# Optimization experiments

Hardware: AMD Instinct MI355X
Metric: run time of the kernel (lower is better)

Reference implementation:

```python
import jax, jax.numpy as jnp
import numpy as np
from jax import lax

N_CLASS = 20
N_BOX = 2
GRID = 56          # n_cell_hw derived from input width: 56*56*(2*5+20) = 94080
BATCH = 256
SCORE_THRESH = 0.1 # hard-coded in _preds_filte
IOU_THRESH = 0.4   # hard-coded in _preds_filte
MAX_OUT = 30       # max_output_size
NMS_CAND = 256     # pre-select top candidates per image before O(K^2) NMS


def setup_inputs() -> dict:
    key = jax.random.key(0)
    D = GRID * GRID * (N_BOX * 5 + N_CLASS)
    net_outs = jax.random.uniform(key, (BATCH, D), dtype=jnp.float32)
    return {"net_outs": net_outs}


def _decode(net_outs):
    # Faithful port of _net_outs_parse (wh_sqrt=True)
    B = net_outs.shape[0]
    S, nb, C = GRID, N_BOX, N_CLASS
    bd1 = C * S * S
    bd2 = bd1 + nb * S * S
    cell_c = net_outs[:, :bd1].reshape(B, S, S, C)
    conf = net_outs[:, bd1:bd2].reshape(B, S, S, nb)
    coord = net_outs[:, bd2:].reshape(B, S, S, nb, 4)
    t_xy, t_wh = coord[..., :2], coord[..., 2:]
    # mesh_grid: w_index varies along axis 1, h_index along axis 0, stacked as (w, h)
    X, Y = jnp.meshgrid(jnp.arange(S, dtype=net_outs.dtype),
                        jnp.arange(S, dtype=net_outs.dtype), indexing='xy')
    grid = jnp.stack([X, Y], axis=-1)[:, :, None, :]  # [S,S,1,2]
    xy = (t_xy + grid) / S
    wh = jnp.square(t_wh)  # wh_sqrt=True
    mn = xy - wh * 0.5
    mx = xy + wh * 0.5
    # boxes_corner = [ymin, xmin, ymax, xmax]
    corners = jnp.concatenate([mn[..., 1:2], mn[..., 0:1], mx[..., 1:2], mx[..., 0:1]], axis=-1)
    c_probs = jnp.broadcast_to(cell_c[:, :, :, None, :], (B, S, S, nb, C))
    return jnp.concatenate([corners, conf[..., None], c_probs], axis=-1)  # [B,S,S,nb,5+C]


def _pairwise_iou(b):
    ymin, xmin, ymax, xmax = b[:, 0], b[:, 1], b[:, 2], b[:, 3]
    area = jnp.maximum(ymax - ymin, 0.0) * jnp.maximum(xmax - xmin, 0.0)
    iy = jnp.maximum(0.0, jnp.minimum(ymax[:, None], ymax[None, :]) - jnp.maximum(ymin[:, None], ymin[None, :]))
    ix = jnp.maximum(0.0, jnp.minimum(xmax[:, None], xmax[None, :]) - jnp.maximum(xmin[:, None], xmin[None, :]))
    inter = iy * ix
    union = area[:, None] + area[None, :] - inter
    return jnp.where(union > 0.0, inter / union, 0.0)


def _nms_image(item):
    # item: [N, 6] = (ymin, xmin, ymax, xmax, score, class)
    scores = item[:, 4]
    _, top_i = lax.top_k(scores, NMS_CAND)   # candidate pre-selection (greedy NMS only ever picks highest scores)
    cand = item[top_i]                       # [K, 6]
    iou = _pairwise_iou(cand[:, :4])         # [K, K]
    neg = jnp.finfo(item.dtype).min

    def step(valid, _):
        m = jnp.where(valid, cand[:, 4], neg)
        idx = jnp.argmax(m)
        ok = valid[idx]
        valid = valid & (iou[idx] <= IOU_THRESH)
        valid = valid.at[idx].set(False)
        return valid, (idx, ok)

    _, (idxs, ok) = lax.scan(step, jnp.ones(NMS_CAND, dtype=bool), None, length=MAX_OUT)
    rows = cand[idxs] * ok[:, None].astype(item.dtype)  # invalid slots -> zero rows (== pad with 0)
    _, oi = lax.top_k(rows[:, 4], MAX_OUT)               # sort by score desc, like tf.nn.top_k on padded preds
    return rows[oi]


def reference(net_outs):
    preds = _decode(net_outs)                    # [B,S,S,nb,25]
    B = preds.shape[0]
    cls_score = preds[..., 4:5] * preds[..., 5:]  # conf * class probs  [B,S,S,nb,C]
    cls = jnp.argmax(cls_score, axis=-1).astype(preds.dtype)
    s = jnp.max(cls_score, axis=-1)
    s = jnp.where(s >= SCORE_THRESH, s, 0.0)
    items = jnp.concatenate([preds[..., :4], s[..., None], cls[..., None]], axis=-1)
    items = items.reshape(B, -1, 6)              # [B, S*S*nb, 6]
    return jax.vmap(_nms_image)(items)           # [B, MAX_OUT, 6]
```

## Files before the change

### kernel.cpp

```cpp
#include <hip/hip_runtime.h>
#include <stdint.h>

#define S      56
#define NC     20
#define NCELL  (S*S)
#define NBOXES (NCELL*2)
#define DIM    94080
#define BD1    62720
#define BD2    68992
#define CAND   256
#define MAXOUT 30
#define NTHR   1024
#define NWAVE  16
#define NBIN   8192
#define CAP    512

__global__ __launch_bounds__(NTHR) void det_kernel(const float* __restrict__ in,
                                                   float* __restrict__ out) {
#pragma clang fp contract(off)
    const int b    = blockIdx.x;
    const int tid  = threadIdx.x;
    const int lane = tid & 63;
    const int wv   = tid >> 6;
    const float* img = in + (size_t)b * DIM;

    __shared__ uint32_t hist[NBIN];
    __shared__ uint32_t wsum[NWAVE];
    __shared__ int      bstar_s;
    __shared__ int      nsel;
    __shared__ uint64_t skey[CAP];
    __shared__ uint64_t ssort[CAND];
    __shared__ float cymin[CAND], cxmin[CAND], cymax[CAND], cxmax[CAND];
    __shared__ float carea[CAND], cscore[CAND], ccls[CAND];
    __shared__ int   klist[MAXOUT];
    __shared__ float rowbuf[MAXOUT * 6];

    ((uint4*)hist)[tid]        = uint4{0,0,0,0};
    ((uint4*)hist)[tid + NTHR] = uint4{0,0,0,0};
    if (tid == 0) nsel = 0;
    if (tid < MAXOUT) klist[tid] = -1;

    uint64_t key[4][2];
    bool     vld[4];
    #pragma unroll
    for (int i = 0; i < 4; i++) {
        int cell = tid + NTHR * i;
        vld[i] = (cell < NCELL);
        key[i][0] = key[i][1] = 0;
        if (vld[i]) {
            const float4* pv = (const float4*)(img + cell * NC);
            float p[NC];
            #pragma unroll
            for (int q = 0; q < 5; q++) {
                float4 v = pv[q];
                p[4*q+0] = v.x; p[4*q+1] = v.y; p[4*q+2] = v.z; p[4*q+3] = v.w;
            }
            float2 cf = *(const float2*)(img + BD1 + cell * 2);
            #pragma unroll
            for (int bb = 0; bb < 2; bb++) {
                float conf = bb ? cf.y : cf.x;
                float best = conf * p[0];
                int   cls  = 0;
                #pragma unroll
                for (int c = 1; c < NC; c++) {
                    float v = conf * p[c];
                    if (v > best) { best = v; cls = c; }
                }
                uint32_t sb = (best >= 0.1f) ? __float_as_uint(best) : 0u;
                int idx = cell * 2 + bb;
                key[i][bb] = ((uint64_t)sb << 18) | ((uint64_t)(8191 - idx) << 5)
                           | (uint64_t)cls;
            }
        }
    }
    __syncthreads();

    #pragma unroll
    for (int i = 0; i < 4; i++) {
        #pragma unroll
        for (int bb = 0; bb < 2; bb++) {
            uint32_t sb = (uint32_t)(key[i][bb] >> 18);
            if (vld[i] && sb != 0u) atomicAdd(&hist[sb >> 17], 1u);
            unsigned long long zm = __ballot(vld[i] && sb == 0u);
            if (lane == 0 && zm) atomicAdd(&hist[0], (uint32_t)__popcll(zm));
        }
    }
    __syncthreads();

    uint4 h0 = ((const uint4*)hist)[2*tid];
    uint4 h1 = ((const uint4*)hist)[2*tid+1];
    uint32_t hsum = h0.x+h0.y+h0.z+h0.w + h1.x+h1.y+h1.z+h1.w;
    uint32_t v = hsum;
    #pragma unroll
    for (int off = 1; off < 64; off <<= 1) {
        uint32_t u = __shfl_down(v, off);
        if (lane + off < 64) v += u;
    }
    if (lane == 0) wsum[wv] = v;
    __syncthreads();
    uint32_t add = 0;
    for (int w = wv + 1; w < NWAVE; w++) add += wsum[w];
    uint32_t Sm    = v + add;
    uint32_t above = Sm - hsum;
    if (above < CAND && CAND <= Sm) {
        uint32_t hh[8] = {h1.w, h1.z, h1.y, h1.x, h0.w, h0.z, h0.y, h0.x};
        uint32_t g = above;
        int bsel = 8 * tid;
        #pragma unroll
        for (int j = 0; j < 8; j++) {
            if (g + hh[j] >= CAND) { bsel = 8 * tid + (7 - j); break; }
            g += hh[j];
        }
        bstar_s = bsel;
    }
    __syncthreads();
    const uint32_t bstar = (uint32_t)bstar_s;

    #pragma unroll
    for (int i = 0; i < 4; i++) {
        #pragma unroll
        for (int bb = 0; bb < 2; bb++) {
            bool pred = vld[i] && ((uint32_t)(key[i][bb] >> 35) >= bstar);
            unsigned long long mask = __ballot(pred);
            if (mask) {
                int leader = __ffsll(mask) - 1;
                int base = 0;
                if (lane == leader) base = atomicAdd(&nsel, (int)__popcll(mask));
                base = __shfl(base, leader);
                if (pred) {
                    int pos = base + (int)__popcll(mask & ((1ull << lane) - 1ull));
                    if (pos < CAP) skey[pos] = key[i][bb];
                }
            }
        }
    }
    __syncthreads();

    const int M = (nsel < CAP) ? nsel : CAP;
    if (tid < M) {
        uint64_t my = skey[tid];
        int r = 0;
        #pragma unroll 4
        for (int j = 0; j < M; j++) r += (skey[j] > my);
        if (r < CAND) ssort[r] = my;
    }
    __syncthreads();

    if (tid < CAND) {
        uint64_t k = ssort[tid];
        int idx      = 8191 - (int)((k >> 5) & 0x1FFF);
        int cls      = (int)(k & 31u);
        uint32_t sb  = (uint32_t)(k >> 18);
        int cell = idx >> 1, bb = idx & 1;
        int i = cell / S, j = cell - i * S;
        float4 co = *(const float4*)(img + BD2 + cell * 8 + bb * 4);
        float x  = (co.x + (float)j) / 56.0f;
        float y  = (co.y + (float)i) / 56.0f;
        float wx = co.z * co.z;
        float wy = co.w * co.w;
        float hx = wx * 0.5f, hy = wy * 0.5f;
        float xmin = x - hx, ymin = y - hy, xmax = x + hx, ymax = y + hy;
        cymin[tid] = ymin; cxmin[tid] = xmin; cymax[tid] = ymax; cxmax[tid] = xmax;
        carea[tid] = fmaxf(ymax - ymin, 0.0f) * fmaxf(xmax - xmin, 0.0f);
        cscore[tid] = __uint_as_float(sb);
        ccls[tid]   = (float)cls;
    }
    __syncthreads();

    if (wv == 0) {
        float bym[4], bxm[4], byM[4], bxM[4], bar[4];
        #pragma unroll
        for (int s = 0; s < 4; s++) {
            int c = 4 * lane + s;
            bym[s] = cymin[c]; bxm[s] = cxmin[c];
            byM[s] = cymax[c]; bxM[s] = cxmax[c]; bar[s] = carea[c];
        }
        unsigned vmask = 0xFu;
        for (int it = 0; it < MAXOUT; it++) {
            unsigned long long mk = __ballot(vmask != 0u);
            if (!mk) break;
            int l0 = __ffsll(mk) - 1;
            int vb = __shfl((int)vmask, l0);
            int p  = 4 * l0 + (__ffs(vb) - 1);
            if (lane == 0) klist[it] = p;
            float pym = cymin[p], pxm = cxmin[p];
            float pyM = cymax[p], pxM = cxmax[p], par = carea[p];
            #pragma unroll
            for (int s = 0; s < 4; s++) {
                int c = 4 * lane + s;
                float iy = fmaxf(0.0f, fminf(pyM, byM[s]) - fmaxf(pym, bym[s]));
                float ix = fmaxf(0.0f, fminf(pxM, bxM[s]) - fmaxf(pxm, bxm[s]));
                float inter = iy * ix;
                float uni   = par + bar[s] - inter;
                float iou   = (uni > 0.0f) ? (inter / uni) : 0.0f;
                if (c == p || !(iou <= 0.4f)) vmask &= ~(1u << s);
            }
        }
    }
    __syncthreads();

    if (tid < MAXOUT) {
        int p = klist[tid];
        float* r = &rowbuf[tid * 6];
        if (p >= 0) {
            r[0] = cymin[p]; r[1] = cxmin[p]; r[2] = cymax[p];
            r[3] = cxmax[p]; r[4] = cscore[p]; r[5] = ccls[p];
        } else {
            r[0] = r[1] = r[2] = r[3] = r[4] = r[5] = 0.0f;
        }
    }
    __syncthreads();
    float* ob = out + (size_t)b * (MAXOUT * 6);
    if (tid < MAXOUT * 6) ob[tid] = rowbuf[tid];
}

extern "C" void kernel_launch(void* const* d_in, const int* in_sizes, int n_in,
                              void* d_out, int out_size, void* d_ws, size_t ws_size,
                              hipStream_t stream) {
    const float* in  = (const float*)d_in[0];
    float*       out = (float*)d_out;
    const int B = in_sizes[0] / DIM;
    det_kernel<<<dim3(B), dim3(NTHR), 0, stream>>>(in, out);
}
```

Measured before the change: 160.1 us.

## Split decode into separate many-block kernel writing keys to workspace

Moves the per-cell class-score decode and key packing out of the single per-image block into a separate kernel that uses eight 256-thread blocks per image and writes 64-bit keys to the workspace buffer. The NMS kernel then reads the precomputed keys and runs histogram selection, sort and suppression as before. The aim is to spread the bandwidth-heavy decode over more blocks than the batch size of 256 allows, so the GPU's compute units are better occupied. In exchange it adds a second launch and a global round trip for roughly 12.8 MB of keys.

```diff
diff --git a/kernel.cpp b/kernel.cpp
--- a/kernel.cpp
+++ b/kernel.cpp
@@ -3,19 +3,63 @@
 
 #define S      56
 #define NC     20
-#define NCELL  (S*S)
-#define NBOXES (NCELL*2)
+#define NCELL  3136
+#define NBOXES 6272
 #define DIM    94080
 #define BD1    62720
 #define BD2    68992
 #define CAND   256
 #define MAXOUT 30
-#define NTHR   1024
-#define NWAVE  16
 #define NBIN   8192
 #define CAP    512
-
-__global__ __launch_bounds__(NTHR) void det_kernel(const float* __restrict__ in,
+#define ABLK   256
+#define BPI    8
+#define CPB    392
+
+__global__ __launch_bounds__(ABLK) void decode_kernel(const float* __restrict__ in,
+                                                      uint64_t* __restrict__ keys) {
+#pragma clang fp contract(off)
+    const int blk = blockIdx.x;
+    const int img = blk >> 3;
+    const int sub = blk & 7;
+    const float* im = in + (size_t)img * DIM;
+    uint64_t* kout = keys + (size_t)img * NBOXES;
+    const int base = sub * CPB;
+    #pragma unroll
+    for (int i = 0; i < 2; i++) {
+        int t = threadIdx.x + ABLK * i;
+        if (t >= CPB) break;
+        int cell = base + t;
+        const float4* pv = (const float4*)(im + cell * NC);
+        float p[NC];
+        #pragma unroll
+        for (int q = 0; q < 5; q++) {
+            float4 v = pv[q];
+            p[4*q+0] = v.x; p[4*q+1] = v.y; p[4*q+2] = v.z; p[4*q+3] = v.w;
+        }
+        float2 cf = *(const float2*)(im + BD1 + cell * 2);
+        uint64_t kk[2];
+        #pragma unroll
+        for (int bb = 0; bb < 2; bb++) {
+            float conf = bb ? cf.y : cf.x;
+            float best = conf * p[0];
+            int   cls  = 0;
+            #pragma unroll
+            for (int c = 1; c < NC; c++) {
+                float v = conf * p[c];
+                if (v > best) { best = v; cls = c; }
+            }
+            uint32_t sb = (best >= 0.1f) ? __float_as_uint(best) : 0u;
+            int idx = cell * 2 + bb;
+            kk[bb] = ((uint64_t)sb << 18) | ((uint64_t)(8191 - idx) << 5) | (uint64_t)cls;
+        }
+        ulonglong2 st; st.x = kk[0]; st.y = kk[1];
+        *(ulonglong2*)(kout + 2 * cell) = st;
+    }
+}
+
+__global__ __launch_bounds__(1024) void nms_kernel(const float* __restrict__ in,
+                                                   const uint64_t* __restrict__ keys,
                                                    float* __restrict__ out) {
 #pragma clang fp contract(off)
     const int b    = blockIdx.x;
@@ -23,9 +67,10 @@
     const int lane = tid & 63;
     const int wv   = tid >> 6;
     const float* img = in + (size_t)b * DIM;
+    const uint64_t* kin = keys + (size_t)b * NBOXES;
 
     __shared__ uint32_t hist[NBIN];
-    __shared__ uint32_t wsum[NWAVE];
+    __shared__ uint32_t wsum[16];
     __shared__ int      bstar_s;
     __shared__ int      nsel;
     __shared__ uint64_t skey[CAP];
@@ -36,54 +81,26 @@
     __shared__ float rowbuf[MAXOUT * 6];
 
     ((uint4*)hist)[tid]        = uint4{0,0,0,0};
-    ((uint4*)hist)[tid + NTHR] = uint4{0,0,0,0};
+    ((uint4*)hist)[tid + 1024] = uint4{0,0,0,0};
     if (tid == 0) nsel = 0;
     if (tid < MAXOUT) klist[tid] = -1;
 
-    uint64_t key[4][2];
-    bool     vld[4];
-    #pragma unroll
-    for (int i = 0; i < 4; i++) {
-        int cell = tid + NTHR * i;
-        vld[i] = (cell < NCELL);
-        key[i][0] = key[i][1] = 0;
-        if (vld[i]) {
-            const float4* pv = (const float4*)(img + cell * NC);
-            float p[NC];
-            #pragma unroll
-            for (int q = 0; q < 5; q++) {
-                float4 v = pv[q];
-                p[4*q+0] = v.x; p[4*q+1] = v.y; p[4*q+2] = v.z; p[4*q+3] = v.w;
-            }
-            float2 cf = *(const float2*)(img + BD1 + cell * 2);
-            #pragma unroll
-            for (int bb = 0; bb < 2; bb++) {
-                float conf = bb ? cf.y : cf.x;
-                float best = conf * p[0];
-                int   cls  = 0;
-                #pragma unroll
-                for (int c = 1; c < NC; c++) {
-                    float v = conf * p[c];
-                    if (v > best) { best = v; cls = c; }
-                }
-                uint32_t sb = (best >= 0.1f) ? __float_as_uint(best) : 0u;
-                int idx = cell * 2 + bb;
-                key[i][bb] = ((uint64_t)sb << 18) | ((uint64_t)(8191 - idx) << 5)
-                           | (uint64_t)cls;
-            }
-        }
-    }
-    __syncthreads();
-
-    #pragma unroll
-    for (int i = 0; i < 4; i++) {
-        #pragma unroll
-        for (int bb = 0; bb < 2; bb++) {
-            uint32_t sb = (uint32_t)(key[i][bb] >> 18);
-            if (vld[i] && sb != 0u) atomicAdd(&hist[sb >> 17], 1u);
-            unsigned long long zm = __ballot(vld[i] && sb == 0u);
-            if (lane == 0 && zm) atomicAdd(&hist[0], (uint32_t)__popcll(zm));
-        }
+    uint64_t key[7];
+    bool     vld[7];
+    #pragma unroll
+    for (int i = 0; i < 7; i++) {
+        int j = tid + 1024 * i;
+        vld[i] = (j < NBOXES);
+        key[i] = vld[i] ? kin[j] : 0;
+    }
+    __syncthreads();
+
+    #pragma unroll
+    for (int i = 0; i < 7; i++) {
+        uint32_t sb = (uint32_t)(key[i] >> 18);
+        if (vld[i] && sb != 0u) atomicAdd(&hist[sb >> 17], 1u);
+        unsigned long long zm = __ballot(vld[i] && sb == 0u);
+        if (lane == 0 && zm) atomicAdd(&hist[0], (uint32_t)__popcll(zm));
     }
     __syncthreads();
 
@@ -99,7 +116,7 @@
     if (lane == 0) wsum[wv] = v;
     __syncthreads();
     uint32_t add = 0;
-    for (int w = wv + 1; w < NWAVE; w++) add += wsum[w];
+    for (int w = wv + 1; w < 16; w++) add += wsum[w];
     uint32_t Sm    = v + add;
     uint32_t above = Sm - hsum;
     if (above < CAND && CAND <= Sm) {
@@ -117,20 +134,17 @@
     const uint32_t bstar = (uint32_t)bstar_s;
 
     #pragma unroll
-    for (int i = 0; i < 4; i++) {
-        #pragma unroll
-        for (int bb = 0; bb < 2; bb++) {
-            bool pred = vld[i] && ((uint32_t)(key[i][bb] >> 35) >= bstar);
-            unsigned long long mask = __ballot(pred);
-            if (mask) {
-                int leader = __ffsll(mask) - 1;
-                int base = 0;
-                if (lane == leader) base = atomicAdd(&nsel, (int)__popcll(mask));
-                base = __shfl(base, leader);
-                if (pred) {
-                    int pos = base + (int)__popcll(mask & ((1ull << lane) - 1ull));
-                    if (pos < CAP) skey[pos] = key[i][bb];
-                }
+    for (int i = 0; i < 7; i++) {
+        bool pred = vld[i] && ((uint32_t)(key[i] >> 35) >= bstar);
+        unsigned long long mask = __ballot(pred);
+        if (mask) {
+            int leader = __ffsll(mask) - 1;
+            int base = 0;
+            if (lane == leader) base = atomicAdd(&nsel, (int)__popcll(mask));
+            base = __shfl(base, leader);
+            if (pred) {
+                int pos = base + (int)__popcll(mask & ((1ull << lane) - 1ull));
+                if (pos < CAP) skey[pos] = key[i];
             }
         }
     }
@@ -219,6 +233,8 @@
                               hipStream_t stream) {
     const float* in  = (const float*)d_in[0];
     float*       out = (float*)d_out;
+    uint64_t*    keys = (uint64_t*)d_ws;
     const int B = in_sizes[0] / DIM;
-    det_kernel<<<dim3(B), dim3(NTHR), 0, stream>>>(in, out);
+    decode_kernel<<<dim3(B * BPI), dim3(ABLK), 0, stream>>>(in, keys);
+    nms_kernel<<<dim3(B), dim3(1024), 0, stream>>>(in, keys, out);
 }
```

After: 161.9 us. Within noise of the previous version (+1.2%).
